# Optimization experiments

Hardware: AMD Instinct MI355X
Metric: run time of the kernel (lower is better)

Reference implementation:

```python
import jax, jax.numpy as jnp
import numpy as np

N_NODES = 100000
N_EDGES = 800000
IN_F, H_F, OUT_F = 512, 256, 64
N_EXPERTS = 4  # k = 1


def _normalize_edges(edge_index, n):
    """gcn_norm: add self loops, symmetric D^-1/2 A D^-1/2 edge weights."""
    loop = jnp.arange(n, dtype=edge_index.dtype)
    row = jnp.concatenate([edge_index[0], loop])
    col = jnp.concatenate([edge_index[1], loop])
    w = jnp.ones(row.shape[0], dtype=jnp.float32)
    deg = jax.ops.segment_sum(w, col, num_segments=n)  # in-degree incl. self loop
    dinv = jnp.where(deg > 0, deg ** -0.5, 0.0)
    norm = dinv[row] * w * dinv[col]
    return row, col, norm


def _propagate(x, row, col, norm, n):
    # message x_j * edge_weight, scatter-add at destination col
    msgs = x[row] * norm[:, None]
    return jax.ops.segment_sum(msgs, col, num_segments=n)


def _moe_linear(x, w_gate, expert_w, expert_b):
    # eval-mode noisy top-k gating with k=1: clean logits, top-1, softmax over
    # a single logit -> gate value 1.0 for the selected expert.
    logits = x @ w_gate                         # [N, E]
    idx = jnp.argmax(logits, axis=-1)           # [N]
    gates = jax.nn.one_hot(idx, N_EXPERTS, dtype=x.dtype)  # [N, E]
    y_all = jnp.einsum('ni,eio->neo', x, expert_w) + expert_b[None]  # [N, E, H]
    return jnp.einsum('ne,neo->no', gates, y_all)


def setup_inputs() -> dict:
    key = jax.random.key(0)
    ks = jax.random.split(key, 8)
    x = jax.random.normal(ks[0], (N_NODES, IN_F), dtype=jnp.float32)
    edge_index = jax.random.randint(ks[1], (2, N_EDGES), 0, N_NODES, dtype=jnp.int64)
    w_gate = jax.random.normal(ks[2], (IN_F, N_EXPERTS), dtype=jnp.float32) * 0.05
    expert_w = jax.random.normal(ks[3], (N_EXPERTS, IN_F, H_F), dtype=jnp.float32) * (1.0 / np.sqrt(IN_F))
    expert_b = jnp.zeros((N_EXPERTS, H_F), dtype=jnp.float32)
    bias1 = jnp.zeros((H_F,), dtype=jnp.float32)
    w2 = jax.random.normal(ks[4], (H_F, OUT_F), dtype=jnp.float32) * (1.0 / np.sqrt(H_F))
    bias2 = jnp.zeros((OUT_F,), dtype=jnp.float32)
    return {"x": x, "edge_index": edge_index, "w_gate": w_gate,
            "expert_w": expert_w, "expert_b": expert_b, "bias1": bias1,
            "w2": w2, "bias2": bias2}


def reference(x, edge_index, w_gate, expert_w, expert_b, bias1, w2, bias2):
    n = x.shape[0]
    row, col, norm = _normalize_edges(edge_index, n)
    # conv1: MoE linear -> propagate -> bias
    h = _moe_linear(x, w_gate, expert_w, expert_b)
    h = _propagate(h, row, col, norm, n) + bias1
    h = jax.nn.relu(h)
    # dropout is identity at eval
    # conv2: plain GCNConv
    h = h @ w2
    h = _propagate(h, row, col, norm, n) + bias2
    return jax.nn.log_softmax(h, axis=1)
```

## Files before the change

kernel.cpp:

```cpp
#include <hip/hip_runtime.h>
#include <math.h>

typedef __bf16 bf16x8 __attribute__((ext_vector_type(8)));
typedef float f32x16 __attribute__((ext_vector_type(16)));

__device__ __forceinline__ float wave_reduce_sum(float v) {
  #pragma unroll
  for (int off = 32; off > 0; off >>= 1) v += __shfl_xor(v, off, 64);
  return v;
}
__device__ __forceinline__ unsigned short f2bf(float f) {
  union { float f; unsigned int u; } v; v.f = f;
  unsigned int r = (v.u + 0x7FFFu + ((v.u >> 16) & 1u)) >> 16;
  return (unsigned short)r;
}
__device__ __forceinline__ float bf2f(unsigned short u) {
  union { unsigned int u; float f; } v; v.u = ((unsigned int)u) << 16;
  return v.f;
}
__device__ __forceinline__ void bf2x(unsigned int u, float& lo, float& hi) {
  union { unsigned int u; float f; } a, b;
  a.u = u << 16; b.u = u & 0xFFFF0000u;
  lo = a.f; hi = b.f;
}

__global__ void k_init(int* cnt, int* meta, int N) {
  int i = blockIdx.x * blockDim.x + threadIdx.x;
  if (i < N) cnt[i] = 0;
  if (i < 32) meta[i] = 0;
}

__global__ void k_count(const int* __restrict__ col, int* __restrict__ cnt, int E) {
  int e = blockIdx.x * blockDim.x + threadIdx.x;
  if (e < E) atomicAdd(&cnt[col[e]], 1);
}

__global__ __launch_bounds__(256) void k_scanA(const int* __restrict__ cnt,
                                               int* __restrict__ incl,
                                               int* __restrict__ bsums, int N) {
  __shared__ int s[1024];
  int base = blockIdx.x * 1024;
  #pragma unroll
  for (int t = 0; t < 4; ++t) {
    int i = threadIdx.x + t * 256;
    int idx = base + i;
    s[i] = (idx < N) ? cnt[idx] : 0;
  }
  __syncthreads();
  for (int d = 1; d < 1024; d <<= 1) {
    int v[4];
    #pragma unroll
    for (int t = 0; t < 4; ++t) {
      int i = threadIdx.x + t * 256;
      v[t] = (i >= d) ? s[i - d] : 0;
    }
    __syncthreads();
    #pragma unroll
    for (int t = 0; t < 4; ++t) {
      int i = threadIdx.x + t * 256;
      s[i] += v[t];
    }
    __syncthreads();
  }
  #pragma unroll
  for (int t = 0; t < 4; ++t) {
    int i = threadIdx.x + t * 256;
    int idx = base + i;
    if (idx < N) incl[idx] = s[i];
  }
  if (threadIdx.x == 0) bsums[blockIdx.x] = s[1023];
}

__global__ __launch_bounds__(256) void k_scanB(const int* __restrict__ bsums,
                                               int* __restrict__ boff, int nb) {
  __shared__ int s[1024];
  #pragma unroll
  for (int t = 0; t < 4; ++t) {
    int i = threadIdx.x + t * 256;
    s[i] = (i < nb) ? bsums[i] : 0;
  }
  __syncthreads();
  for (int d = 1; d < 1024; d <<= 1) {
    int v[4];
    #pragma unroll
    for (int t = 0; t < 4; ++t) {
      int i = threadIdx.x + t * 256;
      v[t] = (i >= d) ? s[i - d] : 0;
    }
    __syncthreads();
    #pragma unroll
    for (int t = 0; t < 4; ++t) {
      int i = threadIdx.x + t * 256;
      s[i] += v[t];
    }
    __syncthreads();
  }
  #pragma unroll
  for (int t = 0; t < 4; ++t) {
    int i = threadIdx.x + t * 256;
    if (i < nb) boff[i] = (i == 0) ? 0 : s[i - 1];
  }
}

__global__ void k_scanC(const int* __restrict__ cnt, const int* __restrict__ incl,
                        const int* __restrict__ boff, int* __restrict__ rowptr,
                        int* __restrict__ cursor, float* __restrict__ dinv, int N, int E) {
  int i = blockIdx.x * blockDim.x + threadIdx.x;
  if (i < N) {
    int ex = incl[i] - cnt[i] + boff[i >> 10];
    rowptr[i] = ex;
    cursor[i] = ex;
    dinv[i] = rsqrtf((float)(cnt[i] + 1));
    if (i == 0) rowptr[N] = E;
  }
}

__global__ void k_scatter(const int* __restrict__ row, const int* __restrict__ col,
                          int* __restrict__ cursor, int* __restrict__ csr, int E) {
  int e = blockIdx.x * blockDim.x + threadIdx.x;
  if (e < E) {
    int c = col[e];
    int p = atomicAdd(&cursor[c], 1);
    csr[p] = row[e];
  }
}

__global__ __launch_bounds__(256) void k_gate(const float* __restrict__ x,
                                              const float* __restrict__ wg,
                                              int* __restrict__ eidx,
                                              int* __restrict__ meta,
                                              unsigned short* __restrict__ xb, int N) {
  __shared__ int lhist[4];
  int tid = threadIdx.x;
  if (tid < 4) lhist[tid] = 0;
  __syncthreads();
  int node = blockIdx.x * 16 + (tid >> 4);
  int sl = tid & 15;
  if (node < N) {
    const float* xr = x + (size_t)node * 512;
    unsigned short* xbr = xb + (size_t)node * 512;
    float l0 = 0.f, l1 = 0.f, l2 = 0.f, l3 = 0.f;
    #pragma unroll
    for (int j = 0; j < 8; ++j) {
      int q = sl + 16 * j;
      float4 xv = *(const float4*)(xr + 4 * q);
      ushort4 ov;
      ov.x = f2bf(xv.x); ov.y = f2bf(xv.y); ov.z = f2bf(xv.z); ov.w = f2bf(xv.w);
      *(ushort4*)(xbr + 4 * q) = ov;
      float4 w0 = *(const float4*)(wg + 4 * (4 * q + 0));
      float4 w1 = *(const float4*)(wg + 4 * (4 * q + 1));
      float4 w2 = *(const float4*)(wg + 4 * (4 * q + 2));
      float4 w3 = *(const float4*)(wg + 4 * (4 * q + 3));
      l0 += xv.x * w0.x + xv.y * w1.x + xv.z * w2.x + xv.w * w3.x;
      l1 += xv.x * w0.y + xv.y * w1.y + xv.z * w2.y + xv.w * w3.y;
      l2 += xv.x * w0.z + xv.y * w1.z + xv.z * w2.z + xv.w * w3.z;
      l3 += xv.x * w0.w + xv.y * w1.w + xv.z * w2.w + xv.w * w3.w;
    }
    #pragma unroll
    for (int off = 8; off > 0; off >>= 1) {
      l0 += __shfl_xor(l0, off, 64);
      l1 += __shfl_xor(l1, off, 64);
      l2 += __shfl_xor(l2, off, 64);
      l3 += __shfl_xor(l3, off, 64);
    }
    if (sl == 0) {
      int a = 0; float best = l0;
      if (l1 > best) { best = l1; a = 1; }
      if (l2 > best) { best = l2; a = 2; }
      if (l3 > best) { best = l3; a = 3; }
      eidx[node] = a;
      atomicAdd(&lhist[a], 1);
    }
  }
  __syncthreads();
  if (tid < 4 && lhist[tid] > 0) atomicAdd(&meta[tid], lhist[tid]);
}

__global__ void k_offs(int* meta) {
  if (threadIdx.x == 0 && blockIdx.x == 0) {
    int* hist = meta;
    int* eoff = meta + 4;
    int* toff = meta + 9;
    int* ecur = meta + 14;
    int s = 0, t = 0;
    eoff[0] = 0; toff[0] = 0;
    for (int e = 0; e < 4; ++e) {
      s += hist[e];
      eoff[e + 1] = s;
      t += (hist[e] + 127) / 128;
      toff[e + 1] = t;
      ecur[e] = eoff[e];
    }
  }
}

__global__ __launch_bounds__(256) void k_binscatter(const int* __restrict__ eidx,
                                                    int* __restrict__ meta,
                                                    int* __restrict__ perm, int N) {
  __shared__ int lhist[4];
  __shared__ int lbase[4];
  int tid = threadIdx.x;
  if (tid < 4) lhist[tid] = 0;
  __syncthreads();
  int n = blockIdx.x * 256 + tid;
  int e = 0, lrank = 0;
  bool valid = (n < N);
  if (valid) {
    e = eidx[n];
    lrank = atomicAdd(&lhist[e], 1);
  }
  __syncthreads();
  if (tid < 4) {
    int c = lhist[tid];
    lbase[tid] = (c > 0) ? atomicAdd(&meta[14 + tid], c) : 0;
  }
  __syncthreads();
  if (valid) perm[lbase[e] + lrank] = n;
}

__global__ __launch_bounds__(256) void k_pack(const float* __restrict__ ew,
                                              unsigned short* __restrict__ ewb) {
  int b = blockIdx.x;
  int n = threadIdx.x;
  int e = b >> 6, kc = b & 63;
  const float* src = ew + ((size_t)e * 512 + (size_t)kc * 8) * 256 + n;
  unsigned short tmp[8];
  #pragma unroll
  for (int ke = 0; ke < 8; ++ke) tmp[ke] = f2bf(src[(size_t)ke * 256]);
  *(uint4*)(ewb + ((size_t)b * 256 + n) * 8) = *(const uint4*)tmp;
}

__global__ __launch_bounds__(64) void k_pack2(const float* __restrict__ w2,
                                              unsigned short* __restrict__ w2b) {
  int kc = blockIdx.x;
  int n = threadIdx.x;
  const float* src = w2 + (size_t)kc * 8 * 64 + n;
  unsigned short tmp[8];
  #pragma unroll
  for (int ke = 0; ke < 8; ++ke) tmp[ke] = f2bf(src[(size_t)ke * 64]);
  *(uint4*)(w2b + ((size_t)kc * 64 + n) * 8) = *(const uint4*)tmp;
}

__global__ __launch_bounds__(512, 2) void k_gemm1(const unsigned short* __restrict__ xb,
                                                  const unsigned short* __restrict__ ewb,
                                                  const float* __restrict__ eb,
                                                  const int* __restrict__ perm,
                                                  const int* __restrict__ meta,
                                                  unsigned short* __restrict__ h1) {
  __shared__ __align__(16) unsigned short A_lds[8192];
  __shared__ __align__(16) unsigned short B_lds[16384];
  __shared__ int sperm[128];
  const int* eoff = meta + 4;
  const int* toff = meta + 9;
  int v = blockIdx.x;
  if (v >= toff[4]) return;
  int e = 0;
  while (v >= toff[e + 1]) ++e;
  int m0 = eoff[e] + (v - toff[e]) * 128;
  int mEnd = eoff[e + 1];
  int tid = threadIdx.x;

  if (tid < 128) {
    int m = m0 + tid;
    sperm[tid] = perm[(m < mEnd) ? m : (mEnd - 1)];
  }
  __syncthreads();

  int wave = tid >> 6, lane = tid & 63;
  int wr = wave >> 2, wc = wave & 3;
  int hi = lane >> 5, lo = lane & 31;

  f32x16 acc[2][2];
  #pragma unroll
  for (int mi = 0; mi < 2; ++mi)
    #pragma unroll
    for (int ni = 0; ni < 2; ++ni)
      #pragma unroll
      for (int r = 0; r < 16; ++r) acc[mi][ni][r] = 0.f;

  const unsigned short* arow = xb + (size_t)sperm[tid & 127] * 512;
  int kclA = tid >> 7;
  const uint4* ebase = (const uint4*)(ewb + (size_t)e * 64 * 2048);

  for (int k0 = 0; k0 < 512; k0 += 64) {
    uint4 a0 = *(const uint4*)(arow + k0 + kclA * 8);
    uint4 a1 = *(const uint4*)(arow + k0 + (kclA + 4) * 8);
    const uint4* bsrc = ebase + (size_t)(k0 >> 3) * 256;
    uint4 b0 = bsrc[tid];
    uint4 b1 = bsrc[512 + tid];
    uint4 b2 = bsrc[1024 + tid];
    uint4 b3 = bsrc[1536 + tid];
    __syncthreads();
    *(uint4*)&A_lds[((size_t)kclA * 128 + (tid & 127)) * 8] = a0;
    *(uint4*)&A_lds[((size_t)(kclA + 4) * 128 + (tid & 127)) * 8] = a1;
    *(uint4*)&B_lds[((size_t)0 * 512 + tid) * 8] = b0;
    *(uint4*)&B_lds[((size_t)1 * 512 + tid) * 8] = b1;
    *(uint4*)&B_lds[((size_t)2 * 512 + tid) * 8] = b2;
    *(uint4*)&B_lds[((size_t)3 * 512 + tid) * 8] = b3;
    __syncthreads();
    #pragma unroll
    for (int s = 0; s < 4; ++s) {
      int kcl = s * 2 + hi;
      bf16x8 a0f = *(const bf16x8*)&A_lds[((size_t)kcl * 128 + wr * 64 + lo) * 8];
      bf16x8 a1f = *(const bf16x8*)&A_lds[((size_t)kcl * 128 + wr * 64 + 32 + lo) * 8];
      bf16x8 b0f = *(const bf16x8*)&B_lds[((size_t)kcl * 256 + wc * 64 + lo) * 8];
      bf16x8 b1f = *(const bf16x8*)&B_lds[((size_t)kcl * 256 + wc * 64 + 32 + lo) * 8];
      acc[0][0] = __builtin_amdgcn_mfma_f32_32x32x16_bf16(a0f, b0f, acc[0][0], 0, 0, 0);
      acc[0][1] = __builtin_amdgcn_mfma_f32_32x32x16_bf16(a0f, b1f, acc[0][1], 0, 0, 0);
      acc[1][0] = __builtin_amdgcn_mfma_f32_32x32x16_bf16(a1f, b0f, acc[1][0], 0, 0, 0);
      acc[1][1] = __builtin_amdgcn_mfma_f32_32x32x16_bf16(a1f, b1f, acc[1][1], 0, 0, 0);
    }
  }

  #pragma unroll
  for (int ni = 0; ni < 2; ++ni) {
    int col = wc * 64 + ni * 32 + lo;
    float bias = eb[e * 256 + col];
    #pragma unroll
    for (int mi = 0; mi < 2; ++mi) {
      #pragma unroll
      for (int q = 0; q < 4; ++q) {
        #pragma unroll
        for (int j = 0; j < 4; ++j) {
          int r = j + 8 * q + 4 * hi;
          int lrow = wr * 64 + mi * 32 + r;
          if (m0 + lrow < mEnd) {
            h1[(size_t)sperm[lrow] * 256 + col] = f2bf(acc[mi][ni][q * 4 + j] + bias);
          }
        }
      }
    }
  }
}

__global__ __launch_bounds__(256) void k_prop1(const unsigned short* __restrict__ h1,
                                               const int* __restrict__ rowptr,
                                               const int* __restrict__ csr,
                                               const float* __restrict__ dinv,
                                               const float* __restrict__ bias1,
                                               unsigned short* __restrict__ hrelu, int N) {
  int tid = threadIdx.x;
  int c = blockIdx.x * 8 + (tid >> 5);
  int l = tid & 31;
  if (c >= N) return;
  float dc = dinv[c];
  const uint4* hr = (const uint4*)h1;
  uint4 sv = hr[(size_t)c * 32 + l];
  float slf = dc * dc;
  float a0, a1, a2, a3, a4, a5, a6, a7;
  {
    float lo, hi;
    bf2x(sv.x, lo, hi); a0 = lo * slf; a1 = hi * slf;
    bf2x(sv.y, lo, hi); a2 = lo * slf; a3 = hi * slf;
    bf2x(sv.z, lo, hi); a4 = lo * slf; a5 = hi * slf;
    bf2x(sv.w, lo, hi); a6 = lo * slf; a7 = hi * slf;
  }
  int jb = rowptr[c], je = rowptr[c + 1];
  int j = jb;
  #define ACC8(v, s) { float lo, hi; \
    bf2x((v).x, lo, hi); a0 += lo * (s); a1 += hi * (s); \
    bf2x((v).y, lo, hi); a2 += lo * (s); a3 += hi * (s); \
    bf2x((v).z, lo, hi); a4 += lo * (s); a5 += hi * (s); \
    bf2x((v).w, lo, hi); a6 += lo * (s); a7 += hi * (s); }
  for (; j + 3 < je; j += 4) {
    int r0 = csr[j], r1 = csr[j + 1], r2 = csr[j + 2], r3 = csr[j + 3];
    float s0 = dinv[r0] * dc, s1 = dinv[r1] * dc, s2 = dinv[r2] * dc, s3 = dinv[r3] * dc;
    uint4 v0 = hr[(size_t)r0 * 32 + l];
    uint4 v1 = hr[(size_t)r1 * 32 + l];
    uint4 v2 = hr[(size_t)r2 * 32 + l];
    uint4 v3 = hr[(size_t)r3 * 32 + l];
    ACC8(v0, s0); ACC8(v1, s1); ACC8(v2, s2); ACC8(v3, s3);
  }
  for (; j < je; ++j) {
    int r = csr[j];
    float s = dinv[r] * dc;
    uint4 v = hr[(size_t)r * 32 + l];
    ACC8(v, s);
  }
  #undef ACC8
  float4 b01 = *(const float4*)(bias1 + l * 8);
  float4 b23 = *(const float4*)(bias1 + l * 8 + 4);
  a0 = fmaxf(a0 + b01.x, 0.f); a1 = fmaxf(a1 + b01.y, 0.f);
  a2 = fmaxf(a2 + b01.z, 0.f); a3 = fmaxf(a3 + b01.w, 0.f);
  a4 = fmaxf(a4 + b23.x, 0.f); a5 = fmaxf(a5 + b23.y, 0.f);
  a6 = fmaxf(a6 + b23.z, 0.f); a7 = fmaxf(a7 + b23.w, 0.f);
  uint4 ov;
  ov.x = ((unsigned int)f2bf(a1) << 16) | f2bf(a0);
  ov.y = ((unsigned int)f2bf(a3) << 16) | f2bf(a2);
  ov.z = ((unsigned int)f2bf(a5) << 16) | f2bf(a4);
  ov.w = ((unsigned int)f2bf(a7) << 16) | f2bf(a6);
  ((uint4*)hrelu)[(size_t)c * 32 + l] = ov;
}

__global__ __launch_bounds__(256, 2) void k_gemm2(const unsigned short* __restrict__ A,
                                                  const unsigned short* __restrict__ w2b,
                                                  unsigned short* __restrict__ h3, int N) {
  __shared__ __align__(16) unsigned short B_lds[16384];
  __shared__ __align__(16) unsigned short A_lds[8192];
  int tid = threadIdx.x;
  int m0 = blockIdx.x * 128;
  #pragma unroll
  for (int it = 0; it < 8; ++it)
    *(uint4*)&B_lds[((size_t)it * 256 + tid) * 8] = ((const uint4*)w2b)[it * 256 + tid];

  int wave = tid >> 6, lane = tid & 63;
  int wr = wave >> 1, wc = wave & 1;
  int hi = lane >> 5, lo = lane & 31;

  f32x16 acc[2];
  #pragma unroll
  for (int mi = 0; mi < 2; ++mi)
    #pragma unroll
    for (int r = 0; r < 16; ++r) acc[mi][r] = 0.f;

  int i = tid & 127;
  int row = m0 + i;
  if (row >= N) row = N - 1;
  const unsigned short* arow = A + (size_t)row * 256;
  int kcl0 = tid >> 7;

  for (int k0 = 0; k0 < 256; k0 += 64) {
    uint4 a[4];
    #pragma unroll
    for (int t = 0; t < 4; ++t)
      a[t] = *(const uint4*)(arow + k0 + (kcl0 + 2 * t) * 8);
    __syncthreads();
    #pragma unroll
    for (int t = 0; t < 4; ++t)
      *(uint4*)&A_lds[((size_t)(kcl0 + 2 * t) * 128 + i) * 8] = a[t];
    __syncthreads();
    #pragma unroll
    for (int s = 0; s < 4; ++s) {
      int kcl = s * 2 + hi;
      bf16x8 a0f = *(const bf16x8*)&A_lds[((size_t)kcl * 128 + wr * 64 + lo) * 8];
      bf16x8 a1f = *(const bf16x8*)&A_lds[((size_t)kcl * 128 + wr * 64 + 32 + lo) * 8];
      bf16x8 bf = *(const bf16x8*)&B_lds[(((size_t)(k0 >> 3) + kcl) * 64 + wc * 32 + lo) * 8];
      acc[0] = __builtin_amdgcn_mfma_f32_32x32x16_bf16(a0f, bf, acc[0], 0, 0, 0);
      acc[1] = __builtin_amdgcn_mfma_f32_32x32x16_bf16(a1f, bf, acc[1], 0, 0, 0);
    }
  }

  int n = wc * 32 + lo;
  #pragma unroll
  for (int mi = 0; mi < 2; ++mi) {
    #pragma unroll
    for (int q = 0; q < 4; ++q) {
      #pragma unroll
      for (int j = 0; j < 4; ++j) {
        int r = j + 8 * q + 4 * hi;
        int orow = m0 + wr * 64 + mi * 32 + r;
        if (orow < N) h3[(size_t)orow * 64 + n] = f2bf(acc[mi][q * 4 + j]);
      }
    }
  }
}

__global__ __launch_bounds__(256) void k_prop2(const unsigned short* __restrict__ h3,
                                               const int* __restrict__ rowptr,
                                               const int* __restrict__ csr,
                                               const float* __restrict__ dinv,
                                               const float* __restrict__ bias2,
                                               float* __restrict__ out, int N) {
  int tid = threadIdx.x;
  int c = blockIdx.x * 32 + (tid >> 3);
  int l = tid & 7;
  if (c >= N) return;
  float dc = dinv[c];
  const uint4* hr = (const uint4*)h3;
  uint4 sv = hr[(size_t)c * 8 + l];
  float slf = dc * dc;
  float a0, a1, a2, a3, a4, a5, a6, a7;
  {
    float lo, hi;
    bf2x(sv.x, lo, hi); a0 = lo * slf; a1 = hi * slf;
    bf2x(sv.y, lo, hi); a2 = lo * slf; a3 = hi * slf;
    bf2x(sv.z, lo, hi); a4 = lo * slf; a5 = hi * slf;
    bf2x(sv.w, lo, hi); a6 = lo * slf; a7 = hi * slf;
  }
  int jb = rowptr[c], je = rowptr[c + 1];
  int j = jb;
  #define ACC8(v, s) { float lo, hi; \
    bf2x((v).x, lo, hi); a0 += lo * (s); a1 += hi * (s); \
    bf2x((v).y, lo, hi); a2 += lo * (s); a3 += hi * (s); \
    bf2x((v).z, lo, hi); a4 += lo * (s); a5 += hi * (s); \
    bf2x((v).w, lo, hi); a6 += lo * (s); a7 += hi * (s); }
  for (; j + 3 < je; j += 4) {
    int r0 = csr[j], r1 = csr[j + 1], r2 = csr[j + 2], r3 = csr[j + 3];
    float s0 = dinv[r0] * dc, s1 = dinv[r1] * dc, s2 = dinv[r2] * dc, s3 = dinv[r3] * dc;
    uint4 v0 = hr[(size_t)r0 * 8 + l];
    uint4 v1 = hr[(size_t)r1 * 8 + l];
    uint4 v2 = hr[(size_t)r2 * 8 + l];
    uint4 v3 = hr[(size_t)r3 * 8 + l];
    ACC8(v0, s0); ACC8(v1, s1); ACC8(v2, s2); ACC8(v3, s3);
  }
  for (; j < je; ++j) {
    int r = csr[j];
    float s = dinv[r] * dc;
    uint4 v = hr[(size_t)r * 8 + l];
    ACC8(v, s);
  }
  #undef ACC8
  float4 b01 = *(const float4*)(bias2 + l * 8);
  float4 b23 = *(const float4*)(bias2 + l * 8 + 4);
  a0 += b01.x; a1 += b01.y; a2 += b01.z; a3 += b01.w;
  a4 += b23.x; a5 += b23.y; a6 += b23.z; a7 += b23.w;
  float m = fmaxf(fmaxf(fmaxf(a0, a1), fmaxf(a2, a3)), fmaxf(fmaxf(a4, a5), fmaxf(a6, a7)));
  #pragma unroll
  for (int off = 4; off > 0; off >>= 1) m = fmaxf(m, __shfl_xor(m, off, 64));
  float s = expf(a0 - m) + expf(a1 - m) + expf(a2 - m) + expf(a3 - m)
          + expf(a4 - m) + expf(a5 - m) + expf(a6 - m) + expf(a7 - m);
  #pragma unroll
  for (int off = 4; off > 0; off >>= 1) s += __shfl_xor(s, off, 64);
  float ls = m + logf(s);
  float* orow = out + (size_t)c * 64 + l * 8;
  float4 o0 = make_float4(a0 - ls, a1 - ls, a2 - ls, a3 - ls);
  float4 o1 = make_float4(a4 - ls, a5 - ls, a6 - ls, a7 - ls);
  *(float4*)orow = o0;
  *(float4*)(orow + 4) = o1;
}

extern "C" void kernel_launch(void* const* d_in, const int* in_sizes, int n_in,
                              void* d_out, int out_size, void* d_ws, size_t ws_size,
                              hipStream_t stream) {
  const float* x  = (const float*)d_in[0];
  const int*   ei = (const int*)d_in[1];
  const float* wg = (const float*)d_in[2];
  const float* ew = (const float*)d_in[3];
  const float* eb = (const float*)d_in[4];
  const float* b1 = (const float*)d_in[5];
  const float* w2 = (const float*)d_in[6];
  const float* b2 = (const float*)d_in[7];
  float* out = (float*)d_out;

  int N = in_sizes[0] / 512;
  int E = in_sizes[1] / 2;
  const int* row = ei;
  const int* col = ei + E;

  char* p = (char*)d_ws;
  auto alloc = [&](size_t bytes) -> void* {
    void* r = (void*)p;
    p += (bytes + 255) & ~(size_t)255;
    return r;
  };
  int*   cnt    = (int*)alloc((size_t)N * 4);
  int*   rowptr = (int*)alloc((size_t)(N + 1) * 4);
  int*   cursor = (int*)alloc((size_t)N * 4);
  int*   bsums  = (int*)alloc(1024 * 4);
  int*   boff   = (int*)alloc(1024 * 4);
  float* dinv   = (float*)alloc((size_t)N * 4);
  int*   eidx   = (int*)alloc((size_t)N * 4);
  int*   meta   = (int*)alloc(32 * 4);
  int*   perm   = (int*)alloc((size_t)N * 4);
  int*   csr    = (int*)alloc((size_t)E * 4);
  unsigned short* h1    = (unsigned short*)alloc((size_t)N * 256 * 2);
  unsigned short* hrelu = (unsigned short*)alloc((size_t)N * 256 * 2);
  unsigned short* h3    = (unsigned short*)alloc((size_t)N * 64 * 2);
  unsigned short* xb  = (unsigned short*)alloc((size_t)N * 512 * 2);
  unsigned short* ewb = (unsigned short*)alloc((size_t)4 * 512 * 256 * 2);
  unsigned short* w2b = (unsigned short*)alloc((size_t)256 * 64 * 2);

  int nb = (N + 1023) / 1024;

  k_init<<<(N + 255) / 256, 256, 0, stream>>>(cnt, meta, N);
  k_count<<<(E + 255) / 256, 256, 0, stream>>>(col, cnt, E);
  k_scanA<<<nb, 256, 0, stream>>>(cnt, rowptr, bsums, N);
  k_scanB<<<1, 256, 0, stream>>>(bsums, boff, nb);
  k_scanC<<<(N + 255) / 256, 256, 0, stream>>>(cnt, rowptr, boff, rowptr, cursor, dinv, N, E);
  k_scatter<<<(E + 255) / 256, 256, 0, stream>>>(row, col, cursor, csr, E);
  k_pack<<<256, 256, 0, stream>>>(ew, ewb);
  k_pack2<<<32, 64, 0, stream>>>(w2, w2b);
  k_gate<<<(N + 15) / 16, 256, 0, stream>>>(x, wg, eidx, meta, xb, N);
  k_offs<<<1, 64, 0, stream>>>(meta);
  k_binscatter<<<(N + 255) / 256, 256, 0, stream>>>(eidx, meta, perm, N);
  int ntiles = (N + 127) / 128 + 4;
  k_gemm1<<<ntiles, 512, 0, stream>>>(xb, ewb, eb, perm, meta, h1);
  k_prop1<<<(N + 7) / 8, 256, 0, stream>>>(h1, rowptr, csr, dinv, b1, hrelu, N);
  k_gemm2<<<(N + 127) / 128, 256, 0, stream>>>(hrelu, w2b, h3, N);
  k_prop2<<<(N + 31) / 32, 256, 0, stream>>>(h3, rowptr, csr, dinv, b2, out, N);
}
```

Before: 395.1 us.

## Use direct global-to-LDS loads in GEMMs, unroll gathers by eight, merge pack kernels

The two GEMM kernels now stage their A and B tiles with global_load_lds, which writes straight into LDS instead of passing through registers. This cuts VGPR use and the separate LDS store instructions. The two propagation kernels gain an 8-way unrolled gather loop that keeps more independent neighbour loads in flight, and the two weight-pack kernels are merged into a single launch. The direct-to-LDS path relies on the compiler inserting the correct waits before the barrier. The loop is still single-buffered, so loads do not overlap with the MFMA work.

```diff
diff --git a/kernel.cpp b/kernel.cpp
--- a/kernel.cpp
+++ b/kernel.cpp
@@ -4,11 +4,6 @@
 typedef __bf16 bf16x8 __attribute__((ext_vector_type(8)));
 typedef float f32x16 __attribute__((ext_vector_type(16)));
 
-__device__ __forceinline__ float wave_reduce_sum(float v) {
-  #pragma unroll
-  for (int off = 32; off > 0; off >>= 1) v += __shfl_xor(v, off, 64);
-  return v;
-}
 __device__ __forceinline__ unsigned short f2bf(float f) {
   union { float f; unsigned int u; } v; v.f = f;
   unsigned int r = (v.u + 0x7FFFu + ((v.u >> 16) & 1u)) >> 16;
@@ -22,6 +17,11 @@
   union { unsigned int u; float f; } a, b;
   a.u = u << 16; b.u = u & 0xFFFF0000u;
   lo = a.f; hi = b.f;
+}
+__device__ __forceinline__ void gload16(const void* g, void* l) {
+  __builtin_amdgcn_global_load_lds(
+      (__attribute__((address_space(1))) void*)const_cast<void*>(g),
+      (__attribute__((address_space(3))) void*)l, 16, 0, 0);
 }
 
 __global__ void k_init(int* cnt, int* meta, int N) {
@@ -219,26 +219,29 @@
 }
 
 __global__ __launch_bounds__(256) void k_pack(const float* __restrict__ ew,
-                                              unsigned short* __restrict__ ewb) {
+                                              unsigned short* __restrict__ ewb,
+                                              const float* __restrict__ w2,
+                                              unsigned short* __restrict__ w2b) {
   int b = blockIdx.x;
-  int n = threadIdx.x;
-  int e = b >> 6, kc = b & 63;
-  const float* src = ew + ((size_t)e * 512 + (size_t)kc * 8) * 256 + n;
-  unsigned short tmp[8];
-  #pragma unroll
-  for (int ke = 0; ke < 8; ++ke) tmp[ke] = f2bf(src[(size_t)ke * 256]);
-  *(uint4*)(ewb + ((size_t)b * 256 + n) * 8) = *(const uint4*)tmp;
-}
-
-__global__ __launch_bounds__(64) void k_pack2(const float* __restrict__ w2,
-                                              unsigned short* __restrict__ w2b) {
-  int kc = blockIdx.x;
-  int n = threadIdx.x;
-  const float* src = w2 + (size_t)kc * 8 * 64 + n;
-  unsigned short tmp[8];
-  #pragma unroll
-  for (int ke = 0; ke < 8; ++ke) tmp[ke] = f2bf(src[(size_t)ke * 64]);
-  *(uint4*)(w2b + ((size_t)kc * 64 + n) * 8) = *(const uint4*)tmp;
+  if (b < 256) {
+    int n = threadIdx.x;
+    int e = b >> 6, kc = b & 63;
+    const float* src = ew + ((size_t)e * 512 + (size_t)kc * 8) * 256 + n;
+    unsigned short tmp[8];
+    #pragma unroll
+    for (int ke = 0; ke < 8; ++ke) tmp[ke] = f2bf(src[(size_t)ke * 256]);
+    *(uint4*)(ewb + ((size_t)b * 256 + n) * 8) = *(const uint4*)tmp;
+  } else {
+    int kc = b - 256;
+    int n = threadIdx.x;
+    if (n < 64) {
+      const float* src = w2 + (size_t)kc * 8 * 64 + n;
+      unsigned short tmp[8];
+      #pragma unroll
+      for (int ke = 0; ke < 8; ++ke) tmp[ke] = f2bf(src[(size_t)ke * 64]);
+      *(uint4*)(w2b + ((size_t)kc * 64 + n) * 8) = *(const uint4*)tmp;
+    }
+  }
 }
 
 __global__ __launch_bounds__(512, 2) void k_gemm1(const unsigned short* __restrict__ xb,
@@ -269,6 +272,7 @@
   int wave = tid >> 6, lane = tid & 63;
   int wr = wave >> 2, wc = wave & 3;
   int hi = lane >> 5, lo = lane & 31;
+  int r128 = tid & 127;
 
   f32x16 acc[2][2];
   #pragma unroll
@@ -278,25 +282,19 @@
       #pragma unroll
       for (int r = 0; r < 16; ++r) acc[mi][ni][r] = 0.f;
 
-  const unsigned short* arow = xb + (size_t)sperm[tid & 127] * 512;
+  const unsigned short* arow = xb + (size_t)sperm[r128] * 512;
   int kclA = tid >> 7;
   const uint4* ebase = (const uint4*)(ewb + (size_t)e * 64 * 2048);
 
   for (int k0 = 0; k0 < 512; k0 += 64) {
-    uint4 a0 = *(const uint4*)(arow + k0 + kclA * 8);
-    uint4 a1 = *(const uint4*)(arow + k0 + (kclA + 4) * 8);
+    __syncthreads();
+    gload16(arow + k0 + kclA * 8,       &A_lds[((size_t)kclA * 128 + r128) * 8]);
+    gload16(arow + k0 + (kclA + 4) * 8, &A_lds[((size_t)(kclA + 4) * 128 + r128) * 8]);
     const uint4* bsrc = ebase + (size_t)(k0 >> 3) * 256;
-    uint4 b0 = bsrc[tid];
-    uint4 b1 = bsrc[512 + tid];
-    uint4 b2 = bsrc[1024 + tid];
-    uint4 b3 = bsrc[1536 + tid];
-    __syncthreads();
-    *(uint4*)&A_lds[((size_t)kclA * 128 + (tid & 127)) * 8] = a0;
-    *(uint4*)&A_lds[((size_t)(kclA + 4) * 128 + (tid & 127)) * 8] = a1;
-    *(uint4*)&B_lds[((size_t)0 * 512 + tid) * 8] = b0;
-    *(uint4*)&B_lds[((size_t)1 * 512 + tid) * 8] = b1;
-    *(uint4*)&B_lds[((size_t)2 * 512 + tid) * 8] = b2;
-    *(uint4*)&B_lds[((size_t)3 * 512 + tid) * 8] = b3;
+    gload16(bsrc + tid,        &B_lds[((size_t)0 * 512 + tid) * 8]);
+    gload16(bsrc + 512 + tid,  &B_lds[((size_t)1 * 512 + tid) * 8]);
+    gload16(bsrc + 1024 + tid, &B_lds[((size_t)2 * 512 + tid) * 8]);
+    gload16(bsrc + 1536 + tid, &B_lds[((size_t)3 * 512 + tid) * 8]);
     __syncthreads();
     #pragma unroll
     for (int s = 0; s < 4; ++s) {
@@ -362,6 +360,19 @@
     bf2x((v).y, lo, hi); a2 += lo * (s); a3 += hi * (s); \
     bf2x((v).z, lo, hi); a4 += lo * (s); a5 += hi * (s); \
     bf2x((v).w, lo, hi); a6 += lo * (s); a7 += hi * (s); }
+  for (; j + 7 < je; j += 8) {
+    int r[8];
+    #pragma unroll
+    for (int t = 0; t < 8; ++t) r[t] = csr[j + t];
+    float s[8];
+    #pragma unroll
+    for (int t = 0; t < 8; ++t) s[t] = dinv[r[t]] * dc;
+    uint4 vv[8];
+    #pragma unroll
+    for (int t = 0; t < 8; ++t) vv[t] = hr[(size_t)r[t] * 32 + l];
+    #pragma unroll
+    for (int t = 0; t < 8; ++t) ACC8(vv[t], s[t]);
+  }
   for (; j + 3 < je; j += 4) {
     int r0 = csr[j], r1 = csr[j + 1], r2 = csr[j + 2], r3 = csr[j + 3];
     float s0 = dinv[r0] * dc, s1 = dinv[r1] * dc, s2 = dinv[r2] * dc, s3 = dinv[r3] * dc;
@@ -401,7 +412,7 @@
   int m0 = blockIdx.x * 128;
   #pragma unroll
   for (int it = 0; it < 8; ++it)
-    *(uint4*)&B_lds[((size_t)it * 256 + tid) * 8] = ((const uint4*)w2b)[it * 256 + tid];
+    gload16(((const uint4*)w2b) + it * 256 + tid, &B_lds[((size_t)it * 256 + tid) * 8]);
 
   int wave = tid >> 6, lane = tid & 63;
   int wr = wave >> 1, wc = wave & 1;
@@ -420,14 +431,11 @@
   int kcl0 = tid >> 7;
 
   for (int k0 = 0; k0 < 256; k0 += 64) {
-    uint4 a[4];
+    __syncthreads();
     #pragma unroll
     for (int t = 0; t < 4; ++t)
-      a[t] = *(const uint4*)(arow + k0 + (kcl0 + 2 * t) * 8);
-    __syncthreads();
-    #pragma unroll
-    for (int t = 0; t < 4; ++t)
-      *(uint4*)&A_lds[((size_t)(kcl0 + 2 * t) * 128 + i) * 8] = a[t];
+      gload16(arow + k0 + (kcl0 + 2 * t) * 8,
+              &A_lds[((size_t)(kcl0 + 2 * t) * 128 + i) * 8]);
     __syncthreads();
     #pragma unroll
     for (int s = 0; s < 4; ++s) {
@@ -484,6 +492,19 @@
     bf2x((v).y, lo, hi); a2 += lo * (s); a3 += hi * (s); \
     bf2x((v).z, lo, hi); a4 += lo * (s); a5 += hi * (s); \
     bf2x((v).w, lo, hi); a6 += lo * (s); a7 += hi * (s); }
+  for (; j + 7 < je; j += 8) {
+    int r[8];
+    #pragma unroll
+    for (int t = 0; t < 8; ++t) r[t] = csr[j + t];
+    float s[8];
+    #pragma unroll
+    for (int t = 0; t < 8; ++t) s[t] = dinv[r[t]] * dc;
+    uint4 vv[8];
+    #pragma unroll
+    for (int t = 0; t < 8; ++t) vv[t] = hr[(size_t)r[t] * 8 + l];
+    #pragma unroll
+    for (int t = 0; t < 8; ++t) ACC8(vv[t], s[t]);
+  }
   for (; j + 3 < je; j += 4) {
     int r0 = csr[j], r1 = csr[j + 1], r2 = csr[j + 2], r3 = csr[j + 3];
     float s0 = dinv[r0] * dc, s1 = dinv[r1] * dc, s2 = dinv[r2] * dc, s3 = dinv[r3] * dc;
@@ -568,8 +589,7 @@
   k_scanB<<<1, 256, 0, stream>>>(bsums, boff, nb);
   k_scanC<<<(N + 255) / 256, 256, 0, stream>>>(cnt, rowptr, boff, rowptr, cursor, dinv, N, E);
   k_scatter<<<(E + 255) / 256, 256, 0, stream>>>(row, col, cursor, csr, E);
-  k_pack<<<256, 256, 0, stream>>>(ew, ewb);
-  k_pack2<<<32, 64, 0, stream>>>(w2, w2b);
+  k_pack<<<288, 256, 0, stream>>>(ew, ewb, w2, w2b);
   k_gate<<<(N + 15) / 16, 256, 0, stream>>>(x, wg, eidx, meta, xb, N);
   k_offs<<<1, 64, 0, stream>>>(meta);
   k_binscatter<<<(N + 255) / 256, 256, 0, stream>>>(eidx, meta, perm, N);
```

Result: no change. 397.3 us (+0.6%).
